# Performance work log

Hardware: AMD Instinct MI355X
Metric: run time of the kernel (lower is better)

The kernel has to match this reference:

```python
import jax, jax.numpy as jnp
import numpy as np

B, L, E, D, H, N_ENT = 64, 50, 50, 100, 100, 200000


def setup_inputs() -> dict:
    key = jax.random.key(0)
    ks = jax.random.split(key, 12)
    neighbor_ids = jax.random.randint(ks[0], (B, L, E), 0, N_ENT)
    # 0/1 adjacency; mimic GraphConstructer: symmetric with self-loops
    adj = jax.random.randint(ks[1], (B, L, E, E), 0, 2).astype(jnp.int32)
    adj = jnp.maximum(adj, adj.transpose(0, 1, 3, 2))
    adj = jnp.maximum(adj, jnp.eye(E, dtype=jnp.int32))
    s = 0.1  # ~ 1/sqrt(D) init scale
    emb = jax.random.normal(ks[2], (N_ENT, D), jnp.float32) * s
    Wq = jax.random.normal(ks[3], (D, H), jnp.float32) * s
    bq = jax.random.normal(ks[4], (H,), jnp.float32) * s
    Wk = jax.random.normal(ks[5], (D, H), jnp.float32) * s
    bk = jax.random.normal(ks[6], (H,), jnp.float32) * s
    Wv = jax.random.normal(ks[7], (D, H), jnp.float32) * s
    bv = jax.random.normal(ks[8], (H,), jnp.float32) * s
    Ws = jax.random.normal(ks[9], (D, H), jnp.float32) * s
    bs = jax.random.normal(ks[10], (H,), jnp.float32) * s
    return {"neighbor_ids": neighbor_ids, "adj": adj, "emb": emb,
            "Wq": Wq, "bq": bq, "Wk": Wk, "bk": bk,
            "Wv": Wv, "bv": bv, "Ws": Ws, "bs": bs}


def reference(neighbor_ids, adj, emb, Wq, bq, Wk, bk, Wv, bv, Ws, bs):
    b, l, e = neighbor_ids.shape
    d = emb.shape[1]
    h = Wq.shape[1]
    # embedding gather: [B,L,E,D] -> [G,E,D], G = B*L graphs
    x = emb[neighbor_ids].reshape(b * l, e, d)
    a = adj.reshape(b * l, e, e)
    # TransformerConv (heads=1): q,k,v linear with bias
    q = x @ Wq + bq
    k = x @ Wk + bk
    v = x @ Wv + bv
    scores = jnp.einsum('gid,gjd->gij', q, k) / jnp.sqrt(jnp.asarray(h, x.dtype))
    # edge (j -> i) exists when adj[j, i] != 0; target i attends over sources j
    mask = a.transpose(0, 2, 1) != 0  # mask[g, i, j]
    neg = jnp.finfo(scores.dtype).min
    attn = jax.nn.softmax(jnp.where(mask, scores, neg), axis=-1)
    # nodes with no incoming edge aggregate to zero (PyG softmax/scatter semantics)
    attn = jnp.where(mask.any(-1, keepdims=True), attn, jnp.zeros((), attn.dtype))
    agg = jnp.einsum('gij,gjd->gid', attn, v)
    out = agg + x @ Ws + bs  # root/skip connection with bias
    # take center node (index 0) of each ego-graph -> [B, L, H]
    return out.reshape(b, l, e, h)[:, :, 0, :]
```

## Files before the change

kernel.cpp:

```cpp
#include <hip/hip_runtime.h>
#include <hip/hip_bf16.h>
#include <math.h>

#define E_N 50
#define D_N 100
#define H_N 100

__device__ __forceinline__ float bf2f(unsigned int s16) {
    return __uint_as_float(s16 << 16);
}

__device__ __forceinline__ unsigned short f2bf(float f) {
    unsigned int u = __float_as_uint(f);
    unsigned int r = (u + 0x7FFFu + ((u >> 16) & 1u)) >> 16;
    return (unsigned short)r;
}

template <bool F32>
__device__ __forceinline__ float ldx(const void* p, int i) {
    if (F32) return reinterpret_cast<const float*>(p)[i];
    return bf2f(reinterpret_cast<const unsigned short*>(p)[i]);
}

template <bool F32>
__device__ __forceinline__ float4 ld4(const void* p, long long i4) {
    if (F32) return reinterpret_cast<const float4*>(p)[i4];
    uint2 v = reinterpret_cast<const uint2*>(p)[i4];
    float4 f;
    f.x = bf2f(v.x & 0xFFFFu);
    f.y = bf2f(v.x >> 16);
    f.z = bf2f(v.y & 0xFFFFu);
    f.w = bf2f(v.y >> 16);
    return f;
}

template <bool F32>
__device__ __forceinline__ void graph_core(
    int g, int tid,
    const int* __restrict__ nbr, const int* __restrict__ adj,
    const void* __restrict__ emb,
    const void* __restrict__ Wq, const void* __restrict__ bq,
    const void* __restrict__ Wk, const void* __restrict__ Wv,
    const void* __restrict__ bv, const void* __restrict__ Ws,
    const void* __restrict__ bs, void* __restrict__ out,
    float* xs, int* ids, int* msk, float* q0s, float* us,
    float* ssc, float* attns, float* ys, float* den_s)
{
    if (tid < E_N) {
        ids[tid] = nbr[g * E_N + tid];
        msk[tid] = adj[(size_t)g * (E_N * E_N) + tid * E_N];
    }
    __syncthreads();

    {
        const int total = E_N * (D_N / 4);
        for (int i = tid; i < total; i += 256) {
            int j  = i / 25;
            int d4 = i - j * 25;
            long long base4 = (long long)ids[j] * (D_N / 4) + d4;
            reinterpret_cast<float4*>(xs)[j * 25 + d4] = ld4<F32>(emb, base4);
        }
    }
    __syncthreads();

    if (tid < H_N) {
        float acc = ldx<F32>(bq, tid);
        for (int d = 0; d < D_N; ++d)
            acc = fmaf(xs[d], ldx<F32>(Wq, d * H_N + tid), acc);
        q0s[tid] = acc;
    }
    __syncthreads();

    if (tid < D_N) {
        float acc = 0.f;
        for (int h = 0; h < H_N; ++h)
            acc = fmaf(ldx<F32>(Wk, tid * H_N + h), q0s[h], acc);
        us[tid] = acc;
    }
    __syncthreads();

    if (tid < E_N) {
        float acc = 0.f;
        const float* xrow = xs + tid * D_N;
        for (int d = 0; d < D_N; ++d)
            acc = fmaf(us[d], xrow[d], acc);
        ssc[tid] = acc * 0.1f;
    }
    __syncthreads();

    float m = -3.0e38f;
    for (int j = 0; j < E_N; ++j)
        if (msk[j]) m = fmaxf(m, ssc[j]);
    if (tid < E_N)
        attns[tid] = msk[tid] ? __expf(ssc[tid] - m) : 0.f;
    __syncthreads();

    if (tid < D_N) {
        float den = 0.f;
        for (int j = 0; j < E_N; ++j) den += attns[j];
        float inv = den > 0.f ? 1.0f / den : 0.f;
        float acc = 0.f;
        for (int j = 0; j < E_N; ++j)
            acc = fmaf(attns[j], xs[j * D_N + tid], acc);
        ys[tid] = acc * inv;
        if (tid == 0) *den_s = den;
    }
    __syncthreads();

    if (tid < H_N) {
        float sflag = *den_s > 0.f ? 1.f : 0.f;
        float acc = ldx<F32>(bs, tid) + ldx<F32>(bv, tid) * sflag;
        for (int d = 0; d < D_N; ++d) {
            acc = fmaf(ys[d], ldx<F32>(Wv, d * H_N + tid), acc);
            acc = fmaf(xs[d], ldx<F32>(Ws, d * H_N + tid), acc);
        }
        size_t o = (size_t)g * H_N + tid;
        if (F32) reinterpret_cast<float*>(out)[o] = acc;
        else     reinterpret_cast<unsigned short*>(out)[o] = f2bf(acc);
    }
}

__global__ __launch_bounds__(256)
void graph_enc_kernel(const int* __restrict__ nbr,
                      const int* __restrict__ adj,
                      const void* __restrict__ emb,
                      const void* __restrict__ Wq, const void* __restrict__ bq,
                      const void* __restrict__ Wk, const void* __restrict__ Wv,
                      const void* __restrict__ bv, const void* __restrict__ Ws,
                      const void* __restrict__ bs, void* __restrict__ out)
{
    const int g = blockIdx.x;
    const int tid = threadIdx.x;

    __shared__ float xs[E_N * D_N];
    __shared__ int   ids[E_N];
    __shared__ int   msk[E_N];
    __shared__ float q0s[H_N];
    __shared__ float us[D_N];
    __shared__ float ssc[E_N];
    __shared__ float attns[E_N];
    __shared__ float ys[D_N];
    __shared__ float den_s;
    __shared__ int   is_f32_s;

    if (tid < 64) {
        unsigned short hw = reinterpret_cast<const unsigned short*>(emb)[tid * 2];
        float v = bf2f(hw);
        float a = fabsf(v);
        int sane = (v == 0.f) || (a >= 1e-4f && a <= 8.0f);
        unsigned long long ball = __ballot(sane);
        if (tid == 0) is_f32_s = (__popcll(ball) < 32) ? 1 : 0;
    }
    __syncthreads();

    if (is_f32_s)
        graph_core<true>(g, tid, nbr, adj, emb, Wq, bq, Wk, Wv, bv, Ws, bs, out,
                         xs, ids, msk, q0s, us, ssc, attns, ys, &den_s);
    else
        graph_core<false>(g, tid, nbr, adj, emb, Wq, bq, Wk, Wv, bv, Ws, bs, out,
                          xs, ids, msk, q0s, us, ssc, attns, ys, &den_s);
}

extern "C" void kernel_launch(void* const* d_in, const int* in_sizes, int n_in,
                              void* d_out, int out_size, void* d_ws, size_t ws_size,
                              hipStream_t stream) {
    const int* nbr = (const int*)d_in[0];
    const int* adj = (const int*)d_in[1];
    const void* emb = d_in[2];
    const void* Wq  = d_in[3];
    const void* bq  = d_in[4];
    const void* Wk  = d_in[5];
    const void* Wv  = d_in[7];
    const void* bv  = d_in[8];
    const void* Ws  = d_in[9];
    const void* bs  = d_in[10];

    const int G = in_sizes[0] / E_N;
    graph_enc_kernel<<<G, 256, 0, stream>>>(nbr, adj, emb, Wq, bq, Wk,
                                            Wv, bv, Ws, bs, d_out);
}
```

Baseline: 187.9 us.

## Precompute Wq·Wk^T in a prep kernel and process two graphs per block

Adds a prep kernel that computes M = Wq·Wk^T, the folded bias vector c, and the combined bias bs+bv into workspace. The per-graph q and k projections then collapse into a single 100x100 matvec on the center node. The main kernel now runs two graphs per 256-thread block with 128 threads each, and stores the gathered neighbor embeddings in LDS as bf16 with padded rows. This is meant to cut per-graph arithmetic and global weight loads and to improve occupancy. It adds a second launch and loses precision on f32 inputs, since x is rounded to bf16 before the score and aggregation steps.

Measured after the change: 191.7 us. 1.02x slower.

```diff
diff --git a/kernel.cpp b/kernel.cpp
--- a/kernel.cpp
+++ b/kernel.cpp
@@ -5,6 +5,7 @@
 #define E_N 50
 #define D_N 100
 #define H_N 100
+#define XS_LD 102
 
 __device__ __forceinline__ float bf2f(unsigned int s16) {
     return __uint_as_float(s16 << 16);
@@ -34,131 +35,200 @@
     return f;
 }
 
-template <bool F32>
-__device__ __forceinline__ void graph_core(
-    int g, int tid,
-    const int* __restrict__ nbr, const int* __restrict__ adj,
-    const void* __restrict__ emb,
-    const void* __restrict__ Wq, const void* __restrict__ bq,
-    const void* __restrict__ Wk, const void* __restrict__ Wv,
-    const void* __restrict__ bv, const void* __restrict__ Ws,
-    const void* __restrict__ bs, void* __restrict__ out,
-    float* xs, int* ids, int* msk, float* q0s, float* us,
-    float* ssc, float* attns, float* ys, float* den_s)
-{
-    if (tid < E_N) {
-        ids[tid] = nbr[g * E_N + tid];
-        msk[tid] = adj[(size_t)g * (E_N * E_N) + tid * E_N];
-    }
-    __syncthreads();
-
-    {
-        const int total = E_N * (D_N / 4);
-        for (int i = tid; i < total; i += 256) {
-            int j  = i / 25;
-            int d4 = i - j * 25;
-            long long base4 = (long long)ids[j] * (D_N / 4) + d4;
-            reinterpret_cast<float4*>(xs)[j * 25 + d4] = ld4<F32>(emb, base4);
-        }
-    }
-    __syncthreads();
-
-    if (tid < H_N) {
-        float acc = ldx<F32>(bq, tid);
-        for (int d = 0; d < D_N; ++d)
-            acc = fmaf(xs[d], ldx<F32>(Wq, d * H_N + tid), acc);
-        q0s[tid] = acc;
-    }
-    __syncthreads();
-
-    if (tid < D_N) {
-        float acc = 0.f;
-        for (int h = 0; h < H_N; ++h)
-            acc = fmaf(ldx<F32>(Wk, tid * H_N + h), q0s[h], acc);
-        us[tid] = acc;
-    }
-    __syncthreads();
-
-    if (tid < E_N) {
-        float acc = 0.f;
-        const float* xrow = xs + tid * D_N;
-        for (int d = 0; d < D_N; ++d)
-            acc = fmaf(us[d], xrow[d], acc);
-        ssc[tid] = acc * 0.1f;
-    }
-    __syncthreads();
-
-    float m = -3.0e38f;
-    for (int j = 0; j < E_N; ++j)
-        if (msk[j]) m = fmaxf(m, ssc[j]);
-    if (tid < E_N)
-        attns[tid] = msk[tid] ? __expf(ssc[tid] - m) : 0.f;
-    __syncthreads();
-
-    if (tid < D_N) {
-        float den = 0.f;
-        for (int j = 0; j < E_N; ++j) den += attns[j];
-        float inv = den > 0.f ? 1.0f / den : 0.f;
-        float acc = 0.f;
-        for (int j = 0; j < E_N; ++j)
-            acc = fmaf(attns[j], xs[j * D_N + tid], acc);
-        ys[tid] = acc * inv;
-        if (tid == 0) *den_s = den;
-    }
-    __syncthreads();
-
-    if (tid < H_N) {
-        float sflag = *den_s > 0.f ? 1.f : 0.f;
-        float acc = ldx<F32>(bs, tid) + ldx<F32>(bv, tid) * sflag;
-        for (int d = 0; d < D_N; ++d) {
-            acc = fmaf(ys[d], ldx<F32>(Wv, d * H_N + tid), acc);
-            acc = fmaf(xs[d], ldx<F32>(Ws, d * H_N + tid), acc);
-        }
-        size_t o = (size_t)g * H_N + tid;
-        if (F32) reinterpret_cast<float*>(out)[o] = acc;
-        else     reinterpret_cast<unsigned short*>(out)[o] = f2bf(acc);
-    }
-}
-
-__global__ __launch_bounds__(256)
-void graph_enc_kernel(const int* __restrict__ nbr,
-                      const int* __restrict__ adj,
-                      const void* __restrict__ emb,
-                      const void* __restrict__ Wq, const void* __restrict__ bq,
-                      const void* __restrict__ Wk, const void* __restrict__ Wv,
-                      const void* __restrict__ bv, const void* __restrict__ Ws,
-                      const void* __restrict__ bs, void* __restrict__ out)
-{
-    const int g = blockIdx.x;
-    const int tid = threadIdx.x;
-
-    __shared__ float xs[E_N * D_N];
-    __shared__ int   ids[E_N];
-    __shared__ int   msk[E_N];
-    __shared__ float q0s[H_N];
-    __shared__ float us[D_N];
-    __shared__ float ssc[E_N];
-    __shared__ float attns[E_N];
-    __shared__ float ys[D_N];
-    __shared__ float den_s;
-    __shared__ int   is_f32_s;
-
+__device__ __forceinline__ int detect_f32(const void* emb, int tid, int* flag_s) {
     if (tid < 64) {
         unsigned short hw = reinterpret_cast<const unsigned short*>(emb)[tid * 2];
         float v = bf2f(hw);
         float a = fabsf(v);
         int sane = (v == 0.f) || (a >= 1e-4f && a <= 8.0f);
         unsigned long long ball = __ballot(sane);
-        if (tid == 0) is_f32_s = (__popcll(ball) < 32) ? 1 : 0;
-    }
-    __syncthreads();
-
-    if (is_f32_s)
-        graph_core<true>(g, tid, nbr, adj, emb, Wq, bq, Wk, Wv, bv, Ws, bs, out,
-                         xs, ids, msk, q0s, us, ssc, attns, ys, &den_s);
+        if (tid == 0) *flag_s = (__popcll(ball) < 32) ? 1 : 0;
+    }
+    __syncthreads();
+    return *flag_s;
+}
+
+template <bool F32>
+__device__ __forceinline__ void prep_core(const void* Wq, const void* bq,
+                                          const void* Wk, const void* bv,
+                                          const void* bs,
+                                          float* Mt, float* c, float* b2,
+                                          int blk, int t) {
+    if (blk < D_N) {
+        if (t < D_N) {
+            float acc = 0.f;
+            #pragma unroll 10
+            for (int h = 0; h < H_N; ++h)
+                acc = fmaf(ldx<F32>(Wk, t * H_N + h), ldx<F32>(Wq, blk * H_N + h), acc);
+            Mt[blk * D_N + t] = acc;
+        }
+    } else {
+        if (t < D_N) {
+            float acc = 0.f;
+            #pragma unroll 10
+            for (int h = 0; h < H_N; ++h)
+                acc = fmaf(ldx<F32>(Wk, t * H_N + h), ldx<F32>(bq, h), acc);
+            c[t] = acc;
+            b2[t] = ldx<F32>(bs, t) + ldx<F32>(bv, t);
+        }
+    }
+}
+
+__global__ __launch_bounds__(128)
+void prep_kernel(const void* __restrict__ emb,
+                 const void* __restrict__ Wq, const void* __restrict__ bq,
+                 const void* __restrict__ Wk, const void* __restrict__ bv,
+                 const void* __restrict__ bs,
+                 float* __restrict__ Mt, float* __restrict__ c,
+                 float* __restrict__ b2) {
+    __shared__ int flag_s;
+    int t = threadIdx.x;
+    int f32 = detect_f32(emb, t, &flag_s);
+    if (f32) prep_core<true>(Wq, bq, Wk, bv, bs, Mt, c, b2, blockIdx.x, t);
+    else     prep_core<false>(Wq, bq, Wk, bv, bs, Mt, c, b2, blockIdx.x, t);
+}
+
+template <bool F32>
+__device__ __forceinline__ void graph_core(
+    int g, int sub, int t,
+    const int* __restrict__ nbr, const int* __restrict__ adj,
+    const void* __restrict__ emb,
+    const void* __restrict__ Wv, const void* __restrict__ Ws,
+    const void* __restrict__ bv,
+    const float* __restrict__ Mt, const float* __restrict__ c,
+    const float* __restrict__ b2, void* __restrict__ out,
+    unsigned short (*xs)[E_N * XS_LD], float (*x0s)[D_N],
+    int (*ids)[E_N], int (*msk)[E_N], float (*us)[D_N],
+    float (*ssc)[E_N], float (*attns)[E_N], float (*ys)[D_N], float* den_s)
+{
+    if (t < E_N) {
+        ids[sub][t] = nbr[g * E_N + t];
+        msk[sub][t] = adj[(size_t)g * (E_N * E_N) + t * E_N];
+    } else if (t >= 64 && t < 64 + 25) {
+        int id0 = nbr[g * E_N];
+        int q = t - 64;
+        float4 f = ld4<F32>(emb, (long long)id0 * (D_N / 4) + q);
+        x0s[sub][4 * q + 0] = f.x;
+        x0s[sub][4 * q + 1] = f.y;
+        x0s[sub][4 * q + 2] = f.z;
+        x0s[sub][4 * q + 3] = f.w;
+    }
+    __syncthreads();
+
+    {
+        unsigned int* xw = reinterpret_cast<unsigned int*>(xs[sub]);
+        for (int i = t; i < E_N * (D_N / 4); i += 128) {
+            int j = i / 25;
+            int q = i - j * 25;
+            float4 f = ld4<F32>(emb, (long long)ids[sub][j] * (D_N / 4) + q);
+            unsigned int w0 = (unsigned int)f2bf(f.x) | ((unsigned int)f2bf(f.y) << 16);
+            unsigned int w1 = (unsigned int)f2bf(f.z) | ((unsigned int)f2bf(f.w) << 16);
+            int wbase = j * (XS_LD / 2) + 2 * q;
+            xw[wbase] = w0;
+            xw[wbase + 1] = w1;
+        }
+    }
+    __syncthreads();
+
+    if (t < D_N) {
+        float acc = c[t];
+        #pragma unroll 10
+        for (int e = 0; e < D_N; ++e)
+            acc = fmaf(Mt[e * D_N + t], x0s[sub][e], acc);
+        us[sub][t] = acc;
+    }
+    __syncthreads();
+
+    if (t < E_N) {
+        const unsigned int* xw = reinterpret_cast<const unsigned int*>(xs[sub])
+                                 + t * (XS_LD / 2);
+        float acc = 0.f;
+        #pragma unroll 10
+        for (int d2 = 0; d2 < D_N / 2; ++d2) {
+            unsigned int w = xw[d2];
+            acc = fmaf(bf2f(w & 0xFFFFu), us[sub][2 * d2], acc);
+            acc = fmaf(bf2f(w >> 16),     us[sub][2 * d2 + 1], acc);
+        }
+        ssc[sub][t] = acc * 0.1f;
+    }
+    __syncthreads();
+
+    if (t < E_N) {
+        float m = -3.0e38f;
+        #pragma unroll 10
+        for (int j = 0; j < E_N; ++j)
+            if (msk[sub][j]) m = fmaxf(m, ssc[sub][j]);
+        attns[sub][t] = msk[sub][t] ? __expf(ssc[sub][t] - m) : 0.f;
+    }
+    __syncthreads();
+
+    if (t < D_N) {
+        float den = 0.f;
+        #pragma unroll 10
+        for (int j = 0; j < E_N; ++j) den += attns[sub][j];
+        float inv = den > 0.f ? 1.0f / den : 0.f;
+        float acc = 0.f;
+        #pragma unroll 10
+        for (int j = 0; j < E_N; ++j) {
+            float xv = bf2f(xs[sub][j * XS_LD + t]);
+            acc = fmaf(attns[sub][j], xv, acc);
+        }
+        ys[sub][t] = acc * inv;
+        if (t == 0) den_s[sub] = den;
+    }
+    __syncthreads();
+
+    if (t < H_N) {
+        float acc = b2[t];
+        if (!(den_s[sub] > 0.f)) acc -= ldx<F32>(bv, t);
+        #pragma unroll 10
+        for (int d = 0; d < D_N; ++d) {
+            acc = fmaf(ys[sub][d],  ldx<F32>(Wv, d * H_N + t), acc);
+            acc = fmaf(x0s[sub][d], ldx<F32>(Ws, d * H_N + t), acc);
+        }
+        size_t o = (size_t)g * H_N + t;
+        if (F32) reinterpret_cast<float*>(out)[o] = acc;
+        else     reinterpret_cast<unsigned short*>(out)[o] = f2bf(acc);
+    }
+}
+
+__global__ __launch_bounds__(256)
+void graph_enc_kernel(const int* __restrict__ nbr,
+                      const int* __restrict__ adj,
+                      const void* __restrict__ emb,
+                      const void* __restrict__ Wv, const void* __restrict__ Ws,
+                      const void* __restrict__ bv,
+                      const float* __restrict__ Mt, const float* __restrict__ c,
+                      const float* __restrict__ b2,
+                      void* __restrict__ out, int G)
+{
+    __shared__ unsigned short xs[2][E_N * XS_LD];
+    __shared__ float x0s[2][D_N];
+    __shared__ int   ids[2][E_N];
+    __shared__ int   msk[2][E_N];
+    __shared__ float us[2][D_N];
+    __shared__ float ssc[2][E_N];
+    __shared__ float attns[2][E_N];
+    __shared__ float ys[2][D_N];
+    __shared__ float den_s[2];
+    __shared__ int   flag_s;
+
+    const int tid = threadIdx.x;
+    const int sub = tid >> 7;
+    const int t   = tid & 127;
+    const int g   = blockIdx.x * 2 + sub;
+
+    int f32 = detect_f32(emb, tid, &flag_s);
+    if (g >= G) {
+        for (int i = 0; i < 6; ++i) __syncthreads();
+        return;
+    }
+    if (f32)
+        graph_core<true>(g, sub, t, nbr, adj, emb, Wv, Ws, bv, Mt, c, b2, out,
+                         xs, x0s, ids, msk, us, ssc, attns, ys, den_s);
     else
-        graph_core<false>(g, tid, nbr, adj, emb, Wq, bq, Wk, Wv, bv, Ws, bs, out,
-                          xs, ids, msk, q0s, us, ssc, attns, ys, &den_s);
+        graph_core<false>(g, sub, t, nbr, adj, emb, Wv, Ws, bv, Mt, c, b2, out,
+                          xs, x0s, ids, msk, us, ssc, attns, ys, den_s);
 }
 
 extern "C" void kernel_launch(void* const* d_in, const int* in_sizes, int n_in,
@@ -175,7 +245,13 @@
     const void* Ws  = d_in[9];
     const void* bs  = d_in[10];
 
+    float* Mt = (float*)d_ws;
+    float* c  = Mt + D_N * D_N;
+    float* b2 = c + D_N;
+
     const int G = in_sizes[0] / E_N;
-    graph_enc_kernel<<<G, 256, 0, stream>>>(nbr, adj, emb, Wq, bq, Wk,
-                                            Wv, bv, Ws, bs, d_out);
-}
+
+    prep_kernel<<<D_N + 1, 128, 0, stream>>>(emb, Wq, bq, Wk, bv, bs, Mt, c, b2);
+    graph_enc_kernel<<<(G + 1) / 2, 256, 0, stream>>>(
+        nbr, adj, emb, Wv, Ws, bv, Mt, c, b2, d_out, G);
+}
```
